# Performance work log

Hardware: AMD Instinct MI355X
Metric: run time of the kernel (lower is better)

Reference implementation:

```python
import jax, jax.numpy as jnp
import numpy as np

N, IN, H, C = 50000, 128, 4, 32
E = 800000
NEG_SLOPE = 0.2


def setup_inputs() -> dict:
    key = jax.random.key(0)
    ks = jax.random.split(key, 8)
    x = jax.random.normal(ks[0], (N, IN), dtype=jnp.float32)
    edge_index = jax.random.randint(ks[1], (2, E), 0, N, dtype=jnp.int64)
    s = 0.1
    W = jax.random.normal(ks[2], (H * C, IN), dtype=jnp.float32) * s
    att_src = jax.random.normal(ks[3], (1, H, C), dtype=jnp.float32) * s
    att_dst = jax.random.normal(ks[4], (1, H, C), dtype=jnp.float32) * s
    bias = jnp.zeros((H * C,), dtype=jnp.float32)
    skip_W = jax.random.normal(ks[5], (H * C, IN), dtype=jnp.float32) * s
    skip_b = jnp.zeros((H * C,), dtype=jnp.float32)
    return {"x": x, "edge_index": edge_index, "W": W, "att_src": att_src,
            "att_dst": att_dst, "bias": bias, "skip_W": skip_W, "skip_b": skip_b}


def reference(x, edge_index, W, att_src, att_dst, bias, skip_W, skip_b):
    src, dst = edge_index[0], edge_index[1]
    # projected node features: [N, H, C]
    xp = (x @ W.T).reshape(N, H, C)
    # per-node attention logits: [N, H]
    a_src = jnp.sum(xp * att_src, axis=-1)
    a_dst = jnp.sum(xp * att_dst, axis=-1)
    # edge logits with LeakyReLU: [E, H]
    e = a_src[src] + a_dst[dst]
    e = jnp.where(e > 0, e, NEG_SLOPE * e)
    # segment softmax over incoming edges of each dst node
    m = jax.ops.segment_max(e, dst, num_segments=N)  # [N, H]
    ex = jnp.exp(e - m[dst])
    denom = jax.ops.segment_sum(ex, dst, num_segments=N)  # [N, H]
    alpha = ex / (denom[dst] + 1e-16)
    # weighted messages and scatter-add aggregation: [N, H, C]
    msg = alpha[:, :, None] * xp[src]
    agg = jax.ops.segment_sum(msg, dst, num_segments=N)
    x_gat = agg.reshape(N, H * C) + bias
    x_skip = x @ skip_W.T + skip_b
    return jax.nn.elu(x_gat + x_skip)
```

## Files before the change

### kernel.cpp

```cpp
#include <hip/hip_runtime.h>
#include <hip/hip_bf16.h>


#define NN 50000
#define EE 800000
#define FD 128
#define NEG_SLOPE 0.2f
#define BKT 64

#define NB_CNT 49
#define NB_CONVW 8
#define NB_MFMA (NN / 16)
#define NB_FILL (EE / 256)

typedef __attribute__((ext_vector_type(8))) short short8;
typedef __attribute__((ext_vector_type(4))) float f32x4;

__device__ inline ushort f2b(float f) {
    __hip_bfloat16 h = __float2bfloat16(f);
    return *reinterpret_cast<ushort*>(&h);
}
__device__ inline float b2f(ushort u) {
    union { float f; unsigned int i; } c;
    c.i = ((unsigned int)u) << 16;
    return c.f;
}

__global__ __launch_bounds__(1024) void gat_init_kernel(
    int* __restrict__ count, const float* __restrict__ W,
    const float* __restrict__ skip_W, ushort* __restrict__ wb)
{
    int b = blockIdx.x;
    if (b < NB_CNT) {
        int i = b * 1024 + threadIdx.x;
        if (i < NN) count[i] = 0;
    } else {
        int i = ((b - NB_CNT) * 1024 + threadIdx.x) * 4;
        int row = i >> 7;
        int colb = i & 127;
        const float* src = (row < 128) ? (W + row * FD + colb)
                                       : (skip_W + (row - 128) * FD + colb);
        float4 v = *reinterpret_cast<const float4*>(src);
        ushort4 o;
        o.x = f2b(v.x); o.y = f2b(v.y); o.z = f2b(v.z); o.w = f2b(v.w);
        *reinterpret_cast<ushort4*>(wb + i) = o;
    }
}

__global__ __launch_bounds__(256) void gat_mfma_fill_kernel(
    const float* __restrict__ x, const ushort* __restrict__ wb,
    const float* __restrict__ att_src, const float* __restrict__ att_dst,
    const float* __restrict__ bias, const float* __restrict__ skip_b,
    ushort* __restrict__ xpb, float* __restrict__ a_src, float* __restrict__ a_dst,
    float* __restrict__ skip,
    const int* __restrict__ idx, int* __restrict__ count, int* __restrict__ colf)
{
    if (blockIdx.x >= NB_MFMA) {
        int k = (blockIdx.x - NB_MFMA) * 256 + threadIdx.x;
        int d = idx[EE + k];
        int r = atomicAdd(&count[d], 1);
        if (r < BKT) colf[d * BKT + r] = idx[k];
        return;
    }

    const int p = blockIdx.x;
    const int tid = threadIdx.x;
    const int w = tid >> 6;
    const int l = tid & 63;
    const int lrow = l & 15;
    const int lgrp = l >> 4;
    const int m0 = p * 16;
    const int is_skip = w >> 1;
    const int ncb = (w & 1) * 64;

    short8 bfrag[4][4];
    const ushort* wbase = wb + (size_t)(is_skip * 128 + ncb) * FD;
    #pragma unroll
    for (int t = 0; t < 4; ++t)
        #pragma unroll
        for (int kk = 0; kk < 4; ++kk)
            bfrag[t][kk] = *reinterpret_cast<const short8*>(
                wbase + (size_t)(t * 16 + lrow) * FD + kk * 32 + lgrp * 8);

    short8 afrag[4];
    const float* xrow = x + (size_t)(m0 + lrow) * FD + lgrp * 8;
    #pragma unroll
    for (int kk = 0; kk < 4; ++kk) {
        float4 a0 = *reinterpret_cast<const float4*>(xrow + kk * 32);
        float4 a1 = *reinterpret_cast<const float4*>(xrow + kk * 32 + 4);
        short8 af;
        af[0] = f2b(a0.x); af[1] = f2b(a0.y); af[2] = f2b(a0.z); af[3] = f2b(a0.w);
        af[4] = f2b(a1.x); af[5] = f2b(a1.y); af[6] = f2b(a1.z); af[7] = f2b(a1.w);
        afrag[kk] = af;
    }

    f32x4 acc[4];
    #pragma unroll
    for (int t = 0; t < 4; ++t) acc[t] = (f32x4){0.f, 0.f, 0.f, 0.f};

    #pragma unroll
    for (int kk = 0; kk < 4; ++kk)
        #pragma unroll
        for (int t = 0; t < 4; ++t)
            acc[t] = __builtin_amdgcn_mfma_f32_16x16x32_bf16(
                afrag[kk], bfrag[t][kk], acc[t], 0, 0, 0);

    if (is_skip) {
        #pragma unroll
        for (int t = 0; t < 4; ++t) {
            int colt = ncb + t * 16 + lrow;
            float add = skip_b[colt] + bias[colt];
            #pragma unroll
            for (int r = 0; r < 4; ++r) {
                int row = m0 + lgrp * 4 + r;
                skip[(size_t)row * FD + colt] = acc[t][r] + add;
            }
        }
    } else {
        float as[4], ad[4];
        #pragma unroll
        for (int t = 0; t < 4; ++t) {
            int colt = ncb + t * 16 + lrow;
            as[t] = att_src[colt];
            ad[t] = att_dst[colt];
            #pragma unroll
            for (int r = 0; r < 4; ++r) {
                int row = m0 + lgrp * 4 + r;
                xpb[(size_t)row * FD + colt] = f2b(acc[t][r]);
            }
        }
        const int h0 = ncb >> 5;
        #pragma unroll
        for (int r = 0; r < 4; ++r) {
            float p0 = acc[0][r] * as[0] + acc[1][r] * as[1];
            float p1 = acc[2][r] * as[2] + acc[3][r] * as[3];
            float q0 = acc[0][r] * ad[0] + acc[1][r] * ad[1];
            float q1 = acc[2][r] * ad[2] + acc[3][r] * ad[3];
            #pragma unroll
            for (int m = 1; m < 16; m <<= 1) {
                p0 += __shfl_xor(p0, m, 64);
                p1 += __shfl_xor(p1, m, 64);
                q0 += __shfl_xor(q0, m, 64);
                q1 += __shfl_xor(q1, m, 64);
            }
            if (lrow == 0) {
                int row = m0 + lgrp * 4 + r;
                a_src[(size_t)row * 4 + h0]     = p0;
                a_src[(size_t)row * 4 + h0 + 1] = p1;
                a_dst[(size_t)row * 4 + h0]     = q0;
                a_dst[(size_t)row * 4 + h0 + 1] = q1;
            }
        }
    }
}

__global__ __launch_bounds__(256) void gat_gather_kernel(
    const int* __restrict__ count, const int* __restrict__ colf,
    const float* __restrict__ a_src, const float* __restrict__ a_dst,
    const ushort* __restrict__ xpb, const float* __restrict__ skip,
    float* __restrict__ out)
{
    int wid = (blockIdx.x * 256 + threadIdx.x) >> 6;
    const int d = __builtin_amdgcn_readfirstlane(wid);
    int lane = threadIdx.x & 63;
    const int h = lane >> 4;
    const int ch = lane * 2;
    const float ad = a_dst[(size_t)d * 4 + h];
    const int beg = d * BKT;
    const int end = beg + count[d];
    float2 sk = *reinterpret_cast<const float2*>(skip + (size_t)d * FD + ch);

    float accx = 0.f, accy = 0.f, asum = 0.f;
    int j = beg;
    for (; j + 4 <= end; j += 4) {
        int s0 = colf[j], s1 = colf[j + 1], s2 = colf[j + 2], s3 = colf[j + 3];
        float e0 = a_src[(size_t)s0 * 4 + h] + ad;
        float e1 = a_src[(size_t)s1 * 4 + h] + ad;
        float e2 = a_src[(size_t)s2 * 4 + h] + ad;
        float e3 = a_src[(size_t)s3 * 4 + h] + ad;
        ushort2 x0 = *reinterpret_cast<const ushort2*>(xpb + (size_t)s0 * FD + ch);
        ushort2 x1 = *reinterpret_cast<const ushort2*>(xpb + (size_t)s1 * FD + ch);
        ushort2 x2 = *reinterpret_cast<const ushort2*>(xpb + (size_t)s2 * FD + ch);
        ushort2 x3 = *reinterpret_cast<const ushort2*>(xpb + (size_t)s3 * FD + ch);
        e0 = e0 > 0.f ? e0 : NEG_SLOPE * e0;
        e1 = e1 > 0.f ? e1 : NEG_SLOPE * e1;
        e2 = e2 > 0.f ? e2 : NEG_SLOPE * e2;
        e3 = e3 > 0.f ? e3 : NEG_SLOPE * e3;
        float p0 = __expf(e0), p1 = __expf(e1), p2 = __expf(e2), p3 = __expf(e3);
        asum += (p0 + p1) + (p2 + p3);
        accx += p0 * b2f(x0.x) + p1 * b2f(x1.x) + p2 * b2f(x2.x) + p3 * b2f(x3.x);
        accy += p0 * b2f(x0.y) + p1 * b2f(x1.y) + p2 * b2f(x2.y) + p3 * b2f(x3.y);
    }
    for (; j < end; ++j) {
        int s = colf[j];
        float e = a_src[(size_t)s * 4 + h] + ad;
        ushort2 xv = *reinterpret_cast<const ushort2*>(xpb + (size_t)s * FD + ch);
        e = e > 0.f ? e : NEG_SLOPE * e;
        float pe = __expf(e);
        asum += pe;
        accx += pe * b2f(xv.x);
        accy += pe * b2f(xv.y);
    }
    float inv = 1.f / (asum + 1e-16f);
    float r0 = sk.x + accx * inv;
    float r1 = sk.y + accy * inv;
    r0 = r0 > 0.f ? r0 : expm1f(r0);
    r1 = r1 > 0.f ? r1 : expm1f(r1);
    *reinterpret_cast<float2*>(out + (size_t)d * FD + ch) = make_float2(r0, r1);
}

extern "C" void kernel_launch(void* const* d_in, const int* in_sizes, int n_in,
                              void* d_out, int out_size, void* d_ws, size_t ws_size,
                              hipStream_t stream)
{
    const float* x       = (const float*)d_in[0];
    const int*   idx     = (const int*)d_in[1];
    const float* W       = (const float*)d_in[2];
    const float* att_src = (const float*)d_in[3];
    const float* att_dst = (const float*)d_in[4];
    const float* bias    = (const float*)d_in[5];
    const float* skip_W  = (const float*)d_in[6];
    const float* skip_b  = (const float*)d_in[7];
    float*       out     = (float*)d_out;

    float*  ws     = (float*)d_ws;
    float*  skip   = ws;
    float*  a_src  = ws + 6400000;
    float*  a_dst  = ws + 6600000;
    int*    count  = (int*)(ws + 6800000);
    int*    colf   = (int*)(ws + 6852000);
    ushort* xpb    = (ushort*)(ws + 10100000);
    ushort* wb     = (ushort*)(ws + 13300000);

    gat_init_kernel<<<NB_CNT + NB_CONVW, 1024, 0, stream>>>(count, W, skip_W, wb);

    gat_mfma_fill_kernel<<<NB_MFMA + NB_FILL, 256, 0, stream>>>(
        x, wb, att_src, att_dst, bias, skip_b, xpb, a_src, a_dst, skip,
        idx, count, colf);

    gat_gather_kernel<<<(NN * 64) / 256, 256, 0, stream>>>(
        count, colf, a_src, a_dst, xpb, skip, out);
}
```

Baseline: 151.1 us.

## Precompute per-edge ranks via atomics in a pre-pass, replace init with memset

Moves the per-destination atomic counting out of the MFMA/fill kernel into a separate pre-kernel that computes and stores each edge's rank, with four edges per thread and vectorized loads and stores. The fill blocks then only read the precomputed rank and scatter the source index. The count array is zeroed with hipMemsetAsync instead of dedicated init blocks. This shortens the fill portion running alongside the MFMA blocks, at the cost of an extra rank array round-trip through memory and one more launch.

```diff
diff --git a/kernel.cpp b/kernel.cpp
--- a/kernel.cpp
+++ b/kernel.cpp
@@ -8,8 +8,8 @@
 #define NEG_SLOPE 0.2f
 #define BKT 64
 
-#define NB_CNT 49
-#define NB_CONVW 8
+#define NB_PRE 782
+#define NB_CONVW 32
 #define NB_MFMA (NN / 16)
 #define NB_FILL (EE / 256)
 
@@ -26,16 +26,24 @@
     return c.f;
 }
 
-__global__ __launch_bounds__(1024) void gat_init_kernel(
-    int* __restrict__ count, const float* __restrict__ W,
-    const float* __restrict__ skip_W, ushort* __restrict__ wb)
+__global__ __launch_bounds__(256) void gat_pre_kernel(
+    const int* __restrict__ idx, int* __restrict__ count, int* __restrict__ rank,
+    const float* __restrict__ W, const float* __restrict__ skip_W,
+    ushort* __restrict__ wb)
 {
     int b = blockIdx.x;
-    if (b < NB_CNT) {
-        int i = b * 1024 + threadIdx.x;
-        if (i < NN) count[i] = 0;
+    if (b < NB_PRE) {
+        int base = (b * 256 + threadIdx.x) * 4;
+        if (base >= EE) return;
+        int4 dd = *reinterpret_cast<const int4*>(idx + EE + base);
+        int4 rr;
+        rr.x = atomicAdd(&count[dd.x], 1);
+        rr.y = atomicAdd(&count[dd.y], 1);
+        rr.z = atomicAdd(&count[dd.z], 1);
+        rr.w = atomicAdd(&count[dd.w], 1);
+        *reinterpret_cast<int4*>(rank + base) = rr;
     } else {
-        int i = ((b - NB_CNT) * 1024 + threadIdx.x) * 4;
+        int i = ((b - NB_PRE) * 256 + threadIdx.x) * 4;
         int row = i >> 7;
         int colb = i & 127;
         const float* src = (row < 128) ? (W + row * FD + colb)
@@ -53,12 +61,12 @@
     const float* __restrict__ bias, const float* __restrict__ skip_b,
     ushort* __restrict__ xpb, float* __restrict__ a_src, float* __restrict__ a_dst,
     float* __restrict__ skip,
-    const int* __restrict__ idx, int* __restrict__ count, int* __restrict__ colf)
+    const int* __restrict__ idx, const int* __restrict__ rank, int* __restrict__ colf)
 {
     if (blockIdx.x >= NB_MFMA) {
         int k = (blockIdx.x - NB_MFMA) * 256 + threadIdx.x;
         int d = idx[EE + k];
-        int r = atomicAdd(&count[d], 1);
+        int r = rank[k];
         if (r < BKT) colf[d * BKT + r] = idx[k];
         return;
     }
@@ -228,15 +236,18 @@
     float*  a_src  = ws + 6400000;
     float*  a_dst  = ws + 6600000;
     int*    count  = (int*)(ws + 6800000);
-    int*    colf   = (int*)(ws + 6852000);
-    ushort* xpb    = (ushort*)(ws + 10100000);
-    ushort* wb     = (ushort*)(ws + 13300000);
-
-    gat_init_kernel<<<NB_CNT + NB_CONVW, 1024, 0, stream>>>(count, W, skip_W, wb);
+    int*    rank   = (int*)(ws + 6852000);
+    int*    colf   = (int*)(ws + 7652000);
+    ushort* xpb    = (ushort*)(ws + 10852000);
+    ushort* wb     = (ushort*)(ws + 14052000);
+
+    hipMemsetAsync(count, 0, (size_t)NN * sizeof(int), stream);
+
+    gat_pre_kernel<<<NB_PRE + NB_CONVW, 256, 0, stream>>>(idx, count, rank, W, skip_W, wb);
 
     gat_mfma_fill_kernel<<<NB_MFMA + NB_FILL, 256, 0, stream>>>(
         x, wb, att_src, att_dst, bias, skip_b, xpb, a_src, a_dst, skip,
-        idx, count, colf);
+        idx, rank, colf);
 
     gat_gather_kernel<<<(NN * 64) / 256, 256, 0, stream>>>(
         count, colf, a_src, a_dst, xpb, skip, out);
```

Result: faster. 129.2 us, median of 2 (-14.5%).
